# Performance work log

Measured on AMD Instinct MI355X. Metric: run time of the kernel, lower is better.

The kernel has to match this reference:

```python
import jax, jax.numpy as jnp
import numpy as np

B = 2048          # batch
D = 256           # agent input dim
S = 32            # num_splines
CANVAS = 128      # canvas_size
NUM_T = 50        # samples along each Bezier curve (hard-coded in module)
BRUSH = 1         # brush_size (hard-coded)
SCALE = 1e-4      # Normal scale hard-coded in forward (log_std is unused)
W_STAMP = -0.07   # per-stamp weight (hard-coded)
BG = 0.3          # background_shade


def setup_inputs() -> dict:
    key = jax.random.key(0)
    k1, k2 = jax.random.split(key, 2)
    x = jax.random.normal(k1, (B, D), dtype=jnp.float32)
    W_agent = jax.random.normal(k2, (D, S * 6), dtype=jnp.float32) * 0.05
    b_agent = jnp.zeros((S * 6,), dtype=jnp.float32)
    return {"x": x, "W_agent": W_agent, "b_agent": b_agent}


def _paint_multiple_splines(sample):
    # sample: [B, S*6] in (0,1)
    bsz = sample.shape[0]
    params = sample.reshape(bsz, -1, 6) * CANVAS          # [B, S, 6]
    P0 = params[..., 0:2][:, :, None, :]                   # [B, S, 1, 2]
    P1 = params[..., 2:4][:, :, None, :]
    P2 = params[..., 4:6][:, :, None, :]
    t = jnp.linspace(0.0, 1.0, NUM_T, dtype=params.dtype).reshape(1, 1, NUM_T, 1)
    # quadratic Bezier: [B, S, T, 2]
    spline_points = (1 - t) ** 2 * P0 + 2 * (1 - t) * t * P1 + t ** 2 * P2
    coords = jnp.round(spline_points).astype(jnp.int32)
    r = jnp.arange(-BRUSH, BRUSH + 1)
    dx, dy = jnp.meshgrid(r, r, indexing="ij")
    dx, dy = dx.ravel(), dy.ravel()                        # [9]
    x_idx = jnp.clip(coords[..., 0][..., None] + dx, 0, CANVAS - 1)  # [B,S,T,9]
    y_idx = jnp.clip(coords[..., 1][..., None] + dy, 0, CANVAS - 1)
    flat_idx = (x_idx * CANVAS + y_idx).reshape(bsz, -1)   # [B, S*T*9]
    weights = jnp.full(flat_idx.shape, W_STAMP, dtype=jnp.float32)
    canvas_flat = jnp.zeros((bsz, CANVAS * CANVAS), dtype=jnp.float32)
    canvas_flat = canvas_flat.at[jnp.arange(bsz)[:, None], flat_idx].add(weights)
    canvas = canvas_flat.reshape(bsz, CANVAS, CANVAS)
    return jnp.clip(canvas + BG, 0.0, 1.0)


def reference(x, W_agent, b_agent):
    mu = x @ W_agent + b_agent                             # [B, S*6]
    scale = jnp.float32(SCALE)
    log2pi = jnp.log(jnp.float32(2.0) * jnp.pi)
    dim = mu.shape[-1]
    # eval-time path: raw_sample = mu
    raw = mu
    log_prob = jnp.sum(
        -0.5 * ((raw - mu) / scale) ** 2 - jnp.log(scale) - 0.5 * log2pi,
        axis=-1,
    )                                                      # [B]
    entropy = jnp.full(
        (mu.shape[0],), dim * (0.5 + 0.5 * log2pi + jnp.log(scale)),
        dtype=jnp.float32,
    )                                                      # [B]
    sample = jax.nn.sigmoid(raw)                           # [B, S*6]
    sketch = _paint_multiple_splines(sample)               # [B, CANVAS, CANVAS]
    return sketch, log_prob, entropy, sample
```

## Files before the change

### kernel.cpp

```cpp
#include <hip/hip_runtime.h>
#include <math.h>

#define NB      2048
#define DIM     256
#define SC6     192
#define CV      128
#define NT      50
#define CWORDS  (CV * CV / 4)

#define LPV  (1591.9491530441301f)
#define ENV  (-1495.9491530441301f)

#define SKETCH_N   ((size_t)NB * CV * CV)
#define LP_OFF     (SKETCH_N)
#define ENT_OFF    (LP_OFF + NB)
#define SAMPLE_OFF (ENT_OFF + NB)

typedef float vfloat4 __attribute__((ext_vector_type(4)));

__device__ __forceinline__ void barrier_lds_only() {
    asm volatile("s_waitcnt lgkmcnt(0)\n\ts_barrier" ::: "memory");
}

__global__ __launch_bounds__(256, 6) void fused_kernel(
    const float* __restrict__ x, const float* __restrict__ W,
    const float* __restrict__ bias, float* __restrict__ out)
{
    __shared__ unsigned int cnt[CWORDS];
    __shared__ double sp[6][32];
    __shared__ double cfa[NT], cfb[NT], cfc[NT];

    const int b   = blockIdx.x;
    const int tid = threadIdx.x;

    if (tid < SC6) {
        const int j = tid;
        const float* xb = x + (size_t)b * DIM;
        double a0 = 0.0, a1 = 0.0;
        #pragma unroll 4
        for (int d = 0; d < DIM; d += 2) {
            a0 = fma((double)xb[d],     (double)W[d * SC6 + j],       a0);
            a1 = fma((double)xb[d + 1], (double)W[(d + 1) * SC6 + j], a1);
        }
        double s0 = 1.0 / (1.0 + exp(-((a0 + a1) + (double)bias[j])));
        out[SAMPLE_OFF + (size_t)b * SC6 + j] = (float)s0;
        sp[j % 6][j / 6] = s0 * 128.0;
    } else {
        const int t2 = tid - SC6;
        uint4* c4 = (uint4*)cnt;
        uint4 z = make_uint4(0u, 0u, 0u, 0u);
        #pragma unroll
        for (int w = t2; w < CWORDS / 4; w += 64) c4[w] = z;
        if (t2 < NT) {
            double t = (t2 == NT - 1) ? 1.0 : (double)t2 * (1.0 / 49.0);
            double u = 1.0 - t;
            cfa[t2] = u * u;
            cfb[t2] = (2.0 * u) * t;
            cfc[t2] = t * t;
        }
        if (t2 == 50) out[LP_OFF  + b] = LPV;
        if (t2 == 51) out[ENT_OFF + b] = ENV;
    }
    barrier_lds_only();

    {
        const int s = tid & 31;
        const double P0x = sp[0][s], P0y = sp[1][s];
        const double P1x = sp[2][s], P1y = sp[3][s];
        const double P2x = sp[4][s], P2y = sp[5][s];

        for (int i = tid; i < 32 * NT; i += 256) {
            int kraw = i >> 5;
            int k    = (kraw * 9) % 50;
            double a  = cfa[k];
            double bq = cfb[k];
            double c  = cfc[k];
            double px = a * P0x + bq * P1x + c * P2x;
            double py = a * P0y + bq * P1y + c * P2y;
            int cx = (int)rint(px);
            int cy = (int)rint(py);

            int y0 = min(max(cy - 1, 0), CV - 1);
            int y1 = min(max(cy,     0), CV - 1);
            int y2 = min(max(cy + 1, 0), CV - 1);
            int cb = y0 >> 2;
            unsigned incA = 1u << ((y0 & 3) << 3);
            unsigned incB = 0u;
            unsigned i1 = 1u << ((y1 & 3) << 3);
            unsigned i2 = 1u << ((y2 & 3) << 3);
            if ((y1 >> 2) == cb) incA += i1; else incB += i1;
            if ((y2 >> 2) == cb) incA += i2; else incB += i2;

            int x0 = min(max(cx - 1, 0), CV - 1);
            int x1 = min(max(cx,     0), CV - 1);
            int x2 = min(max(cx + 1, 0), CV - 1);
            int rows[3] = {x0, x1, x2};
            #pragma unroll
            for (int r = 0; r < 3; ++r) {
                int xi = rows[r];
                int base = xi << 5;
                atomicAdd(&cnt[base + ((cb + xi) & 31)], incA);
                if (incB) atomicAdd(&cnt[base + ((cb + 1 + xi) & 31)], incB);
            }
        }
    }
    barrier_lds_only();

    vfloat4* ob = (vfloat4*)(out + (size_t)b * CV * CV);
    for (int w = tid; w < CWORDS; w += 256) {
        int xi  = w >> 5;
        int idx = (xi << 5) + (((w & 31) + xi) & 31);
        unsigned v = cnt[idx];
        vfloat4 r;
        r.x = fminf(fmaxf(0.3f - 0.07f * (float)( v         & 255u), 0.0f), 1.0f);
        r.y = fminf(fmaxf(0.3f - 0.07f * (float)((v >>  8) & 255u), 0.0f), 1.0f);
        r.z = fminf(fmaxf(0.3f - 0.07f * (float)((v >> 16) & 255u), 0.0f), 1.0f);
        r.w = fminf(fmaxf(0.3f - 0.07f * (float)( v >> 24        ), 0.0f), 1.0f);
        ob[w] = r;
    }
}

extern "C" void kernel_launch(void* const* d_in, const int* in_sizes, int n_in,
                              void* d_out, int out_size, void* d_ws, size_t ws_size,
                              hipStream_t stream) {
    const float* x    = (const float*)d_in[0];
    const float* W    = (const float*)d_in[1];
    const float* bias = (const float*)d_in[2];
    float* out = (float*)d_out;

    fused_kernel<<<NB, 256, 0, stream>>>(x, W, bias, out);
}
```

Measured before the change: 158.6 us.

## Split fused kernel into batched GEMM-sigmoid kernel and separate paint kernel

Moves the fp64 linear layer and sigmoid out of the paint kernel into its own kernel, where each block computes four batch rows so every W load is reused four times. The paint kernel reads the stored float sample back, and all 256 threads now share the canvas zeroing instead of just 64. This removes the long serial dot product from the critical path of each paint block and cuts redundant W traffic. The cost is an extra kernel launch plus a global round trip for the samples. Painting coordinates now come from the float-rounded sample rather than the double value, which could shift rounding at pixel boundaries.

```diff
diff --git a/kernel.cpp b/kernel.cpp
--- a/kernel.cpp
+++ b/kernel.cpp
@@ -22,9 +22,45 @@
     asm volatile("s_waitcnt lgkmcnt(0)\n\ts_barrier" ::: "memory");
 }
 
-__global__ __launch_bounds__(256, 6) void fused_kernel(
+__global__ __launch_bounds__(192) void gemm_kernel(
     const float* __restrict__ x, const float* __restrict__ W,
     const float* __restrict__ bias, float* __restrict__ out)
+{
+    const int b0 = blockIdx.x * 4;
+    const int j  = threadIdx.x;
+    const float* xb = x + (size_t)b0 * DIM;
+
+    double a00 = 0.0, a01 = 0.0, a10 = 0.0, a11 = 0.0;
+    double a20 = 0.0, a21 = 0.0, a30 = 0.0, a31 = 0.0;
+    #pragma unroll 4
+    for (int d = 0; d < DIM; d += 2) {
+        double w0 = (double)W[d * SC6 + j];
+        double w1 = (double)W[(d + 1) * SC6 + j];
+        a00 = fma((double)xb[d],               w0, a00);
+        a01 = fma((double)xb[d + 1],           w1, a01);
+        a10 = fma((double)xb[DIM + d],         w0, a10);
+        a11 = fma((double)xb[DIM + d + 1],     w1, a11);
+        a20 = fma((double)xb[2 * DIM + d],     w0, a20);
+        a21 = fma((double)xb[2 * DIM + d + 1], w1, a21);
+        a30 = fma((double)xb[3 * DIM + d],     w0, a30);
+        a31 = fma((double)xb[3 * DIM + d + 1], w1, a31);
+    }
+    double bj = (double)bias[j];
+    double s0 = 1.0 / (1.0 + exp(-((a00 + a01) + bj)));
+    double s1 = 1.0 / (1.0 + exp(-((a10 + a11) + bj)));
+    double s2 = 1.0 / (1.0 + exp(-((a20 + a21) + bj)));
+    double s3 = 1.0 / (1.0 + exp(-((a30 + a31) + bj)));
+    out[SAMPLE_OFF + (size_t)b0 * SC6 + j]       = (float)s0;
+    out[SAMPLE_OFF + (size_t)(b0 + 1) * SC6 + j] = (float)s1;
+    out[SAMPLE_OFF + (size_t)(b0 + 2) * SC6 + j] = (float)s2;
+    out[SAMPLE_OFF + (size_t)(b0 + 3) * SC6 + j] = (float)s3;
+    if (j < 4) {
+        out[LP_OFF  + b0 + j] = LPV;
+        out[ENT_OFF + b0 + j] = ENV;
+    }
+}
+
+__global__ __launch_bounds__(256, 6) void paint_kernel(float* __restrict__ out)
 {
     __shared__ unsigned int cnt[CWORDS];
     __shared__ double sp[6][32];
@@ -34,23 +70,10 @@
     const int tid = threadIdx.x;
 
     if (tid < SC6) {
-        const int j = tid;
-        const float* xb = x + (size_t)b * DIM;
-        double a0 = 0.0, a1 = 0.0;
-        #pragma unroll 4
-        for (int d = 0; d < DIM; d += 2) {
-            a0 = fma((double)xb[d],     (double)W[d * SC6 + j],       a0);
-            a1 = fma((double)xb[d + 1], (double)W[(d + 1) * SC6 + j], a1);
-        }
-        double s0 = 1.0 / (1.0 + exp(-((a0 + a1) + (double)bias[j])));
-        out[SAMPLE_OFF + (size_t)b * SC6 + j] = (float)s0;
-        sp[j % 6][j / 6] = s0 * 128.0;
+        float sf = out[SAMPLE_OFF + (size_t)b * SC6 + tid];
+        sp[tid % 6][tid / 6] = (double)sf * 128.0;
     } else {
         const int t2 = tid - SC6;
-        uint4* c4 = (uint4*)cnt;
-        uint4 z = make_uint4(0u, 0u, 0u, 0u);
-        #pragma unroll
-        for (int w = t2; w < CWORDS / 4; w += 64) c4[w] = z;
         if (t2 < NT) {
             double t = (t2 == NT - 1) ? 1.0 : (double)t2 * (1.0 / 49.0);
             double u = 1.0 - t;
@@ -58,8 +81,12 @@
             cfb[t2] = (2.0 * u) * t;
             cfc[t2] = t * t;
         }
-        if (t2 == 50) out[LP_OFF  + b] = LPV;
-        if (t2 == 51) out[ENT_OFF + b] = ENV;
+    }
+    {
+        uint4* c4 = (uint4*)cnt;
+        uint4 z = make_uint4(0u, 0u, 0u, 0u);
+        #pragma unroll
+        for (int w = tid; w < CWORDS / 4; w += 256) c4[w] = z;
     }
     barrier_lds_only();
 
@@ -128,5 +155,6 @@
     const float* bias = (const float*)d_in[2];
     float* out = (float*)d_out;
 
-    fused_kernel<<<NB, 256, 0, stream>>>(x, W, bias, out);
+    gemm_kernel<<<NB / 4, SC6, 0, stream>>>(x, W, bias, out);
+    paint_kernel<<<NB, 256, 0, stream>>>(out);
 }
```

Result: slower. 164.2 us (+3.5%).
